# Kernel optimization log

Measured on AMD Instinct MI355X. Metric: run time of the kernel, lower is better.

## Reference

```python
import jax, jax.numpy as jnp
import numpy as np

BN_EPS = 1e-5
LRELU_SLOPE = 0.2


def setup_inputs() -> dict:
    key = jax.random.key(0)
    ks = jax.random.split(key, 8)
    B, N, D = 32, 2048, 64      # batch, nodes per graph, latent_dim
    E = 1_000_000               # num edges
    H = 128                     # edge_hidden_dim
    Din = 2 * D + 4             # concat(z_src, z_dst, edge_attr)
    z = jax.random.normal(ks[0], (B, N, D), dtype=jnp.float32)
    edge_index = jax.random.randint(ks[1], (2, E), 0, B * N, dtype=jnp.int64)
    edge_attr = jax.random.normal(ks[2], (E, 4), dtype=jnp.float32)
    W1 = jax.random.normal(ks[3], (Din, H), dtype=jnp.float32) * (1.0 / np.sqrt(Din))
    b1 = jnp.zeros((H,), dtype=jnp.float32)
    gamma = jnp.ones((H,), dtype=jnp.float32)
    beta = jnp.zeros((H,), dtype=jnp.float32)
    W2 = jax.random.normal(ks[4], (H, 1), dtype=jnp.float32) * (1.0 / np.sqrt(H))
    b2 = jnp.zeros((1,), dtype=jnp.float32)
    return {"z": z, "edge_attr": edge_attr, "W1": W1, "b1": b1,
            "gamma": gamma, "beta": beta, "W2": W2, "b2": b2,
            "edge_index": edge_index}


def reference(z, edge_attr, W1, b1, gamma, beta, W2, b2, edge_index):
    B, N, D = z.shape
    zf = z.reshape(-1, D)                       # [B*N, D]
    src, dst = edge_index[0], edge_index[1]
    edge_batch = jnp.clip(src // N, 0, B - 1)
    edge_offsets = edge_batch * N               # batch_offsets[edge_batch]
    src_idx = src % N + edge_offsets
    dst_idx = dst % N + edge_offsets
    edge_input = jnp.concatenate([zf[src_idx], zf[dst_idx], edge_attr], axis=1)  # [E, 2D+4]
    h = edge_input @ W1 + b1                    # [E, H]
    # BatchNorm1d (training mode: biased batch stats over edge dim)
    mu = jnp.mean(h, axis=0)
    var = jnp.mean(jnp.square(h - mu), axis=0)
    h = (h - mu) * jax.lax.rsqrt(var + BN_EPS) * gamma + beta
    h = jnp.where(h >= 0, h, LRELU_SLOPE * h)   # LeakyReLU(0.2)
    return h @ W2 + b2                          # [E, 1]
```

## Files before the change

kernel.cpp:

```cpp
#include <hip/hip_runtime.h>

#define E_EDGES   1000000
#define NNODES    2048
#define HCH       128
#define KP        136
#define TILE      64
#define NTILES    (E_EDGES / TILE)
#define NSPREAD   8
#define GRID_GEMM 1024
#define BPB       128
#define ZVEC      (32 * 2048 * 64 / 4)
#define ZBLK      2048
#define WBLK      66
#define NBIN      8
#define CBLK      512

typedef short  shortx8 __attribute__((ext_vector_type(8)));
typedef float  floatx4 __attribute__((ext_vector_type(4)));

__device__ __forceinline__ unsigned short f2bf(float f) {
  union { float f; unsigned int u; } v; v.f = f;
  unsigned int r = (v.u + 0x7fffu + ((v.u >> 16) & 1u)) >> 16;
  return (unsigned short)r;
}
__device__ __forceinline__ void cfence() { asm volatile("" ::: "memory"); }
__device__ __forceinline__ void bar_lds() {
  asm volatile("s_waitcnt lgkmcnt(0)" ::: "memory");
  __builtin_amdgcn_s_barrier();
  cfence();
}
__device__ __forceinline__ unsigned pack_rows(int s, int d) {
  unsigned rs = (unsigned)s & 0xFFFFu;
  unsigned rd = (unsigned)(((s & ~(NNODES - 1)) | (d & (NNODES - 1)))) & 0xFFFFu;
  return rs | (rd << 16);
}

__global__ void k_prep(const float* __restrict__ z, const float* __restrict__ W1,
                       const float* __restrict__ b1, const int* __restrict__ ei,
                       unsigned short* __restrict__ zb, unsigned short* __restrict__ w1t,
                       float* __restrict__ gstats, int* __restrict__ cnt) {
  int bid = blockIdx.x;
  if (bid < ZBLK) {
    const float4* z4 = (const float4*)z;
    ushort4* zb4 = (ushort4*)zb;
    for (int i = bid * 256 + threadIdx.x; i < ZVEC; i += ZBLK * 256) {
      float4 v = z4[i];
      ushort4 o;
      o.x = f2bf(v.x); o.y = f2bf(v.y); o.z = f2bf(v.z); o.w = f2bf(v.w);
      zb4[i] = o;
    }
  } else if (bid < ZBLK + WBLK) {
    int idx = (bid - ZBLK) * 256 + threadIdx.x;
    int k = idx >> 7, n = idx & 127;
    w1t[n * KP + k] = f2bf(W1[idx]);
  } else if (bid == ZBLK + WBLK) {
    int tid = threadIdx.x;
    if (tid < 512) {
      int n = tid >> 2, kp = 132 + (tid & 3);
      w1t[n * KP + kp] = (kp == 132) ? f2bf(b1[n]) : (unsigned short)0;
    }
    for (int i = tid; i < NSPREAD * 2 * HCH; i += 256) gstats[i] = 0.f;
  } else {
    __shared__ int lh[NBIN];
    int tid = threadIdx.x;
    int cb = bid - (ZBLK + WBLK + 1);
    if (tid < NBIN) lh[tid] = 0;
    __syncthreads();
    for (int e = cb * 256 + tid; e < E_EDGES; e += CBLK * 256)
      atomicAdd(&lh[((unsigned)ei[e]) >> 13], 1);
    __syncthreads();
    if (tid < NBIN) cnt[cb * NBIN + tid] = lh[tid];
  }
}

__global__ void k_scan(const int* __restrict__ cnt, int* __restrict__ base,
                       int* __restrict__ binTile) {
  __shared__ int tot[NBIN], S[NBIN + 1];
  int b = threadIdx.x;
  if (b < NBIN) {
    int t = 0;
    for (int blk = 0; blk < CBLK; ++blk) t += cnt[blk * NBIN + b];
    tot[b] = t;
  }
  __syncthreads();
  if (b == 0) {
    int a = 0;
    for (int i = 0; i < NBIN; ++i) { S[i] = a; a += tot[i]; }
    S[NBIN] = a;
    binTile[0] = 0;
    for (int i = 1; i <= NBIN; ++i) binTile[i] = (S[i] + 63) >> 6;
  }
  __syncthreads();
  if (b < NBIN) {
    int run = S[b];
    for (int blk = 0; blk < CBLK; ++blk) {
      base[blk * NBIN + b] = run;
      run += cnt[blk * NBIN + b];
    }
  }
}

__global__ __launch_bounds__(256)
void k_scatter(const int* __restrict__ ei, const float* __restrict__ attr,
               const int* __restrict__ base, uint4* __restrict__ recs) {
  __shared__ int lcnt[NBIN];
  int tid = threadIdx.x, bid = blockIdx.x;
  if (tid < NBIN) lcnt[tid] = base[bid * NBIN + tid];
  __syncthreads();
  for (int e = bid * 256 + tid; e < E_EDGES; e += CBLK * 256) {
    int s = ei[e], d = ei[E_EDGES + e];
    float4 a = ((const float4*)attr)[e];
    int b = ((unsigned)s) >> 13;
    int slot = atomicAdd(&lcnt[b], 1);
    uint4 r;
    r.x = pack_rows(s, d);
    r.y = (unsigned)f2bf(a.x) | ((unsigned)f2bf(a.y) << 16);
    r.z = (unsigned)f2bf(a.z) | ((unsigned)f2bf(a.w) << 16);
    r.w = (unsigned)e;
    recs[slot] = r;
  }
}

template<bool OUT>
__global__ __launch_bounds__(256, 4)
void k_gemm(const unsigned short* __restrict__ zb,
            const unsigned short* __restrict__ w1t,
            const uint4* __restrict__ recs,
            const int* __restrict__ binTile,
            float* __restrict__ gstats,
            const float* __restrict__ gamma,
            const float* __restrict__ beta,
            const float* __restrict__ W2,
            const float* __restrict__ b2,
            float* __restrict__ out) {
  __shared__ __align__(16) unsigned short A[2][TILE * KP];
  __shared__ float po[2][4][TILE];
  __shared__ int ostash[3][TILE];

  const int tid  = threadIdx.x;
  const int lane = tid & 63;
  const int w    = tid >> 6;
  const int l15  = lane & 15;
  const int quad = lane >> 4;
  const int ea   = w * 8 + (lane >> 3);
  const int eb   = ea + 32;
  const int ch   = lane & 7;

  shortx8 bfr[2][4], bfr4[2];
#pragma unroll
  for (int nt = 0; nt < 2; ++nt) {
    const unsigned short* bp = w1t + (w * 32 + nt * 16 + l15) * KP;
#pragma unroll
    for (int kk = 0; kk < 4; ++kk)
      bfr[nt][kk] = *(const shortx8*)(bp + kk * 32 + quad * 8);
    bfr4[nt] = (quad == 0) ? *(const shortx8*)(bp + 128)
                           : (shortx8){0, 0, 0, 0, 0, 0, 0, 0};
  }

  float eaf[2], ebb[2], ew2[2], b2v = 0.f;
  float ssum[2] = {0.f, 0.f}, ssq[2] = {0.f, 0.f};
  if (OUT) {
#pragma unroll
    for (int nt = 0; nt < 2; ++nt) {
      int c = w * 32 + nt * 16 + l15;
      float S = 0.f, Q = 0.f;
#pragma unroll
      for (int i = 0; i < NSPREAD; ++i) {
        S += gstats[i * 2 * HCH + c];
        Q += gstats[i * 2 * HCH + HCH + c];
      }
      float mu   = S * (1.0f / (float)E_EDGES);
      float var  = Q * (1.0f / (float)E_EDGES) - mu * mu;
      float rstd = rsqrtf(var + 1e-5f);
      float a = gamma[c] * rstd;
      eaf[nt] = a;
      ebb[nt] = beta[c] - mu * a;
      ew2[nt] = W2[c];
    }
    b2v = b2[0];
  }

  if (tid < 128) {
    int b = tid >> 6, r = tid & 63;
    ushort4 bl; bl.x = 0x3F80; bl.y = 0; bl.z = 0; bl.w = 0;
    *(ushort4*)(&A[b][0] + r * KP + 132) = bl;
  }

  const int x    = blockIdx.x & 7;
  const int t0i  = binTile[x] + (blockIdx.x >> 3);
  const int tEnd = binTile[x + 1];
  if (t0i >= tEnd) return;

  auto stage = [&](uint4 ra, uint4 rb, const uint4& h0, const uint4& h1,
                   const uint4& h2, const uint4& h3, int buf, int os) {
    *(uint4*)(&A[buf][0] + ea * KP + ch * 8)      = h0;
    *(uint4*)(&A[buf][0] + eb * KP + ch * 8)      = h1;
    *(uint4*)(&A[buf][0] + ea * KP + 64 + ch * 8) = h2;
    *(uint4*)(&A[buf][0] + eb * KP + 64 + ch * 8) = h3;
    if (ch == 0) {
      ushort4 aA; aA.x = (unsigned short)ra.y; aA.y = (unsigned short)(ra.y >> 16);
      aA.z = (unsigned short)ra.z; aA.w = (unsigned short)(ra.z >> 16);
      *(ushort4*)(&A[buf][0] + ea * KP + 128) = aA;
      ushort4 aB; aB.x = (unsigned short)rb.y; aB.y = (unsigned short)(rb.y >> 16);
      aB.z = (unsigned short)rb.z; aB.w = (unsigned short)(rb.z >> 16);
      *(ushort4*)(&A[buf][0] + eb * KP + 128) = aB;
      ostash[os][ea] = (int)ra.w;
      ostash[os][eb] = (int)rb.w;
    }
  };

  uint4 g0, g1, g2, g3;
  uint4 recSa, recSb;
  uint4 recFa, recFb;
  {
    uint4 ra = recs[t0i * TILE + ea];
    uint4 rb = recs[t0i * TILE + eb];
    unsigned r0 = ra.x & 0xFFFFu, r1 = rb.x & 0xFFFFu;
    unsigned r2 = ra.x >> 16,     r3 = rb.x >> 16;
    uint4 h0 = *(const uint4*)(zb + (size_t)r0 * 64 + ch * 8);
    uint4 h1 = *(const uint4*)(zb + (size_t)r1 * 64 + ch * 8);
    uint4 h2 = *(const uint4*)(zb + (size_t)r2 * 64 + ch * 8);
    uint4 h3 = *(const uint4*)(zb + (size_t)r3 * 64 + ch * 8);
    stage(ra, rb, h0, h1, h2, h3, 0, 0);
    int t1 = t0i + BPB; if (t1 > tEnd - 1) t1 = tEnd - 1;
    recSa = recs[t1 * TILE + ea];
    recSb = recs[t1 * TILE + eb];
    r0 = recSa.x & 0xFFFFu; r1 = recSb.x & 0xFFFFu;
    r2 = recSa.x >> 16;     r3 = recSb.x >> 16;
    g0 = *(const uint4*)(zb + (size_t)r0 * 64 + ch * 8);
    g1 = *(const uint4*)(zb + (size_t)r1 * 64 + ch * 8);
    g2 = *(const uint4*)(zb + (size_t)r2 * 64 + ch * 8);
    g3 = *(const uint4*)(zb + (size_t)r3 * 64 + ch * 8);
    int t2 = t0i + 2 * BPB; if (t2 > tEnd - 1) t2 = tEnd - 1;
    recFa = recs[t2 * TILE + ea];
    recFb = recs[t2 * TILE + eb];
  }
  bar_lds();

  int pp = 0, sl = 0, osr = 0;
  for (int tile = t0i; ; ) {
    const int tnext = tile + BPB;
    const bool more = tnext < tEnd;
    const int osw = (osr == 2) ? 0 : osr + 1;

    if (more) {
      stage(recSa, recSb, g0, g1, g2, g3, pp ^ 1, osw);
      unsigned r0 = recFa.x & 0xFFFFu, r1 = recFb.x & 0xFFFFu;
      unsigned r2 = recFa.x >> 16,     r3 = recFb.x >> 16;
      g0 = *(const uint4*)(zb + (size_t)r0 * 64 + ch * 8);
      g1 = *(const uint4*)(zb + (size_t)r1 * 64 + ch * 8);
      g2 = *(const uint4*)(zb + (size_t)r2 * 64 + ch * 8);
      g3 = *(const uint4*)(zb + (size_t)r3 * 64 + ch * 8);
      recSa = recFa; recSb = recFb;
      int tn3 = tile + 3 * BPB; if (tn3 > tEnd - 1) tn3 = tEnd - 1;
      recFa = recs[tn3 * TILE + ea];
      recFb = recs[tn3 * TILE + eb];
    }

    const unsigned short* Ar = &A[pp][0];
#pragma unroll
    for (int mt = 0; mt < 4; ++mt) {
      const unsigned short* ap = Ar + (mt * 16 + l15) * KP;
      shortx8 afr[4], a4;
#pragma unroll
      for (int kk = 0; kk < 4; ++kk)
        afr[kk] = *(const shortx8*)(ap + kk * 32 + quad * 8);
      a4 = (quad == 0) ? *(const shortx8*)(ap + 128)
                       : (shortx8){0, 0, 0, 0, 0, 0, 0, 0};

      floatx4 acc[2];
      acc[0] = (floatx4){0.f, 0.f, 0.f, 0.f};
      acc[1] = (floatx4){0.f, 0.f, 0.f, 0.f};
#pragma unroll
      for (int kk = 0; kk < 4; ++kk)
#pragma unroll
        for (int nt = 0; nt < 2; ++nt)
          acc[nt] = __builtin_amdgcn_mfma_f32_16x16x32_bf16(
              afr[kk], bfr[nt][kk], acc[nt], 0, 0, 0);
#pragma unroll
      for (int nt = 0; nt < 2; ++nt)
        acc[nt] = __builtin_amdgcn_mfma_f32_16x16x32_bf16(
            a4, bfr4[nt], acc[nt], 0, 0, 0);

      if (!OUT) {
#pragma unroll
        for (int nt = 0; nt < 2; ++nt) {
          float s = 0.f, qq = 0.f;
#pragma unroll
          for (int r = 0; r < 4; ++r) {
            float h = acc[nt][r];
            s += h; qq += h * h;
          }
          ssum[nt] += s; ssq[nt] += qq;
        }
      } else {
#pragma unroll
        for (int r = 0; r < 4; ++r) {
          float t = 0.f;
#pragma unroll
          for (int nt = 0; nt < 2; ++nt) {
            float h = acc[nt][r];
            float p = fmaf(eaf[nt], h, ebb[nt]);
            p = (p >= 0.f) ? p : 0.2f * p;
            t = fmaf(ew2[nt], p, t);
          }
          t += __shfl_xor(t, 1);
          t += __shfl_xor(t, 2);
          t += __shfl_xor(t, 4);
          t += __shfl_xor(t, 8);
          if (l15 == 0)
            po[sl][w][mt * 16 + quad * 4 + r] = t;
        }
      }
    }

    if (more || OUT) bar_lds();

    if (OUT && tid < TILE)
      out[ostash[osr][tid]] = po[sl][0][tid] + po[sl][1][tid] +
                              po[sl][2][tid] + po[sl][3][tid] + b2v;

    if (!more) break;
    pp ^= 1; sl ^= 1; osr = osw;
    tile = tnext;
  }

  if (!OUT) {
    float* gs = gstats + (blockIdx.x & (NSPREAD - 1)) * 2 * HCH;
#pragma unroll
    for (int nt = 0; nt < 2; ++nt) {
      float s = ssum[nt], qq = ssq[nt];
      s += __shfl_xor(s, 16); s += __shfl_xor(s, 32);
      qq += __shfl_xor(qq, 16); qq += __shfl_xor(qq, 32);
      if (quad == 0) {
        int c = w * 32 + nt * 16 + l15;
        atomicAdd(&gs[c], s);
        atomicAdd(&gs[HCH + c], qq);
      }
    }
  }
}

extern "C" void kernel_launch(void* const* d_in, const int* in_sizes, int n_in,
                              void* d_out, int out_size, void* d_ws, size_t ws_size,
                              hipStream_t stream) {
  const float* z     = (const float*)d_in[0];
  const float* attr  = (const float*)d_in[1];
  const float* W1    = (const float*)d_in[2];
  const float* b1    = (const float*)d_in[3];
  const float* gamma = (const float*)d_in[4];
  const float* beta  = (const float*)d_in[5];
  const float* W2    = (const float*)d_in[6];
  const float* b2    = (const float*)d_in[7];
  const int*   ei    = (const int*)d_in[8];
  float* out = (float*)d_out;

  char* ws = (char*)d_ws;
  unsigned short* zb  = (unsigned short*)ws;
  unsigned short* w1t = (unsigned short*)(ws + 8388608);
  float* gstats       = (float*)(ws + 8423424);
  int* cnt            = (int*)(ws + 8431616);
  int* base           = (int*)(ws + 8448000);
  int* binTile        = (int*)(ws + 8464384);
  uint4* recs         = (uint4*)(ws + 8464448);

  k_prep<<<ZBLK + WBLK + 1 + CBLK, 256, 0, stream>>>(z, W1, b1, ei, zb, w1t,
                                                     gstats, cnt);
  k_scan<<<1, 64, 0, stream>>>(cnt, base, binTile);
  k_scatter<<<CBLK, 256, 0, stream>>>(ei, attr, base, recs);
  k_gemm<false><<<GRID_GEMM, 256, 0, stream>>>(zb, w1t, recs, binTile, gstats,
                                               gamma, beta, W2, b2, nullptr);
  k_gemm<true><<<GRID_GEMM, 256, 0, stream>>>(zb, w1t, recs, binTile, gstats,
                                              gamma, beta, W2, b2, out);
}
```

Before: 261.5 us.

## Load gathered z rows directly into MFMA registers, drop LDS staging

```diff
diff --git a/kernel.cpp b/kernel.cpp
--- a/kernel.cpp
+++ b/kernel.cpp
@@ -23,12 +23,6 @@
   unsigned int r = (v.u + 0x7fffu + ((v.u >> 16) & 1u)) >> 16;
   return (unsigned short)r;
 }
-__device__ __forceinline__ void cfence() { asm volatile("" ::: "memory"); }
-__device__ __forceinline__ void bar_lds() {
-  asm volatile("s_waitcnt lgkmcnt(0)" ::: "memory");
-  __builtin_amdgcn_s_barrier();
-  cfence();
-}
 __device__ __forceinline__ unsigned pack_rows(int s, int d) {
   unsigned rs = (unsigned)s & 0xFFFFu;
   unsigned rd = (unsigned)(((s & ~(NNODES - 1)) | (d & (NNODES - 1)))) & 0xFFFFu;
@@ -38,7 +32,8 @@
 __global__ void k_prep(const float* __restrict__ z, const float* __restrict__ W1,
                        const float* __restrict__ b1, const int* __restrict__ ei,
                        unsigned short* __restrict__ zb, unsigned short* __restrict__ w1t,
-                       float* __restrict__ gstats, int* __restrict__ cnt) {
+                       float* __restrict__ gstats, int* __restrict__ cnt,
+                       float* __restrict__ out) {
   int bid = blockIdx.x;
   if (bid < ZBLK) {
     const float4* z4 = (const float4*)z;
@@ -49,6 +44,9 @@
       o.x = f2bf(v.x); o.y = f2bf(v.y); o.z = f2bf(v.z); o.w = f2bf(v.w);
       zb4[i] = o;
     }
+    float4 zf = {0.f, 0.f, 0.f, 0.f};
+    float4* o4 = (float4*)out;
+    for (int i = bid * 256 + threadIdx.x; i < (E_EDGES / 4); i += ZBLK * 256) o4[i] = zf;
   } else if (bid < ZBLK + WBLK) {
     int idx = (bid - ZBLK) * 256 + threadIdx.x;
     int k = idx >> 7, n = idx & 127;
@@ -133,18 +131,11 @@
             const float* __restrict__ W2,
             const float* __restrict__ b2,
             float* __restrict__ out) {
-  __shared__ __align__(16) unsigned short A[2][TILE * KP];
-  __shared__ float po[2][4][TILE];
-  __shared__ int ostash[3][TILE];
-
   const int tid  = threadIdx.x;
   const int lane = tid & 63;
   const int w    = tid >> 6;
   const int l15  = lane & 15;
   const int quad = lane >> 4;
-  const int ea   = w * 8 + (lane >> 3);
-  const int eb   = ea + 32;
-  const int ch   = lane & 7;
 
   shortx8 bfr[2][4], bfr4[2];
 #pragma unroll
@@ -177,13 +168,7 @@
       ebb[nt] = beta[c] - mu * a;
       ew2[nt] = W2[c];
     }
-    b2v = b2[0];
-  }
-
-  if (tid < 128) {
-    int b = tid >> 6, r = tid & 63;
-    ushort4 bl; bl.x = 0x3F80; bl.y = 0; bl.z = 0; bl.w = 0;
-    *(ushort4*)(&A[b][0] + r * KP + 132) = bl;
+    b2v = (w == 0) ? b2[0] : 0.f;
   }
 
   const int x    = blockIdx.x & 7;
@@ -191,138 +176,83 @@
   const int tEnd = binTile[x + 1];
   if (t0i >= tEnd) return;
 
-  auto stage = [&](uint4 ra, uint4 rb, const uint4& h0, const uint4& h1,
-                   const uint4& h2, const uint4& h3, int buf, int os) {
-    *(uint4*)(&A[buf][0] + ea * KP + ch * 8)      = h0;
-    *(uint4*)(&A[buf][0] + eb * KP + ch * 8)      = h1;
-    *(uint4*)(&A[buf][0] + ea * KP + 64 + ch * 8) = h2;
-    *(uint4*)(&A[buf][0] + eb * KP + 64 + ch * 8) = h3;
-    if (ch == 0) {
-      ushort4 aA; aA.x = (unsigned short)ra.y; aA.y = (unsigned short)(ra.y >> 16);
-      aA.z = (unsigned short)ra.z; aA.w = (unsigned short)(ra.z >> 16);
-      *(ushort4*)(&A[buf][0] + ea * KP + 128) = aA;
-      ushort4 aB; aB.x = (unsigned short)rb.y; aB.y = (unsigned short)(rb.y >> 16);
-      aB.z = (unsigned short)rb.z; aB.w = (unsigned short)(rb.z >> 16);
-      *(ushort4*)(&A[buf][0] + eb * KP + 128) = aB;
-      ostash[os][ea] = (int)ra.w;
-      ostash[os][eb] = (int)rb.w;
-    }
+  const char* zq = (const char*)zb + quad * 16;
+
+  auto zload = [&](uint4 rec, uint4* zf) {
+    unsigned so = (rec.x & 0xFFFFu) << 7;
+    unsigned dofs = (rec.x >> 16) << 7;
+    zf[0] = *(const uint4*)(zq + so);
+    zf[1] = *(const uint4*)(zq + so + 64);
+    zf[2] = *(const uint4*)(zq + dofs);
+    zf[3] = *(const uint4*)(zq + dofs + 64);
   };
 
-  uint4 g0, g1, g2, g3;
-  uint4 recSa, recSb;
-  uint4 recFa, recFb;
-  {
-    uint4 ra = recs[t0i * TILE + ea];
-    uint4 rb = recs[t0i * TILE + eb];
-    unsigned r0 = ra.x & 0xFFFFu, r1 = rb.x & 0xFFFFu;
-    unsigned r2 = ra.x >> 16,     r3 = rb.x >> 16;
-    uint4 h0 = *(const uint4*)(zb + (size_t)r0 * 64 + ch * 8);
-    uint4 h1 = *(const uint4*)(zb + (size_t)r1 * 64 + ch * 8);
-    uint4 h2 = *(const uint4*)(zb + (size_t)r2 * 64 + ch * 8);
-    uint4 h3 = *(const uint4*)(zb + (size_t)r3 * 64 + ch * 8);
-    stage(ra, rb, h0, h1, h2, h3, 0, 0);
-    int t1 = t0i + BPB; if (t1 > tEnd - 1) t1 = tEnd - 1;
-    recSa = recs[t1 * TILE + ea];
-    recSb = recs[t1 * TILE + eb];
-    r0 = recSa.x & 0xFFFFu; r1 = recSb.x & 0xFFFFu;
-    r2 = recSa.x >> 16;     r3 = recSb.x >> 16;
-    g0 = *(const uint4*)(zb + (size_t)r0 * 64 + ch * 8);
-    g1 = *(const uint4*)(zb + (size_t)r1 * 64 + ch * 8);
-    g2 = *(const uint4*)(zb + (size_t)r2 * 64 + ch * 8);
-    g3 = *(const uint4*)(zb + (size_t)r3 * 64 + ch * 8);
-    int t2 = t0i + 2 * BPB; if (t2 > tEnd - 1) t2 = tEnd - 1;
-    recFa = recs[t2 * TILE + ea];
-    recFb = recs[t2 * TILE + eb];
-  }
-  bar_lds();
-
-  int pp = 0, sl = 0, osr = 0;
-  for (int tile = t0i; ; ) {
-    const int tnext = tile + BPB;
-    const bool more = tnext < tEnd;
-    const int osw = (osr == 2) ? 0 : osr + 1;
-
-    if (more) {
-      stage(recSa, recSb, g0, g1, g2, g3, pp ^ 1, osw);
-      unsigned r0 = recFa.x & 0xFFFFu, r1 = recFb.x & 0xFFFFu;
-      unsigned r2 = recFa.x >> 16,     r3 = recFb.x >> 16;
-      g0 = *(const uint4*)(zb + (size_t)r0 * 64 + ch * 8);
-      g1 = *(const uint4*)(zb + (size_t)r1 * 64 + ch * 8);
-      g2 = *(const uint4*)(zb + (size_t)r2 * 64 + ch * 8);
-      g3 = *(const uint4*)(zb + (size_t)r3 * 64 + ch * 8);
-      recSa = recFa; recSb = recFb;
-      int tn3 = tile + 3 * BPB; if (tn3 > tEnd - 1) tn3 = tEnd - 1;
-      recFa = recs[tn3 * TILE + ea];
-      recFb = recs[tn3 * TILE + eb];
-    }
-
-    const unsigned short* Ar = &A[pp][0];
-#pragma unroll
-    for (int mt = 0; mt < 4; ++mt) {
-      const unsigned short* ap = Ar + (mt * 16 + l15) * KP;
-      shortx8 afr[4], a4;
-#pragma unroll
-      for (int kk = 0; kk < 4; ++kk)
-        afr[kk] = *(const shortx8*)(ap + kk * 32 + quad * 8);
-      a4 = (quad == 0) ? *(const shortx8*)(ap + 128)
-                       : (shortx8){0, 0, 0, 0, 0, 0, 0, 0};
-
-      floatx4 acc[2];
-      acc[0] = (floatx4){0.f, 0.f, 0.f, 0.f};
-      acc[1] = (floatx4){0.f, 0.f, 0.f, 0.f};
-#pragma unroll
-      for (int kk = 0; kk < 4; ++kk)
-#pragma unroll
-        for (int nt = 0; nt < 2; ++nt)
-          acc[nt] = __builtin_amdgcn_mfma_f32_16x16x32_bf16(
-              afr[kk], bfr[nt][kk], acc[nt], 0, 0, 0);
+  auto do_mt = [&](uint4 rec, const uint4* zf, int tile, int mt) {
+    int4 ai;
+    if (quad == 0) { ai.x = (int)rec.y; ai.y = (int)rec.z; ai.z = 0x3F80; ai.w = 0; }
+    else           { ai.x = 0; ai.y = 0; ai.z = 0; ai.w = 0; }
+    shortx8 a4; __builtin_memcpy(&a4, &ai, 16);
+
+    floatx4 acc[2];
+    acc[0] = (floatx4){0.f, 0.f, 0.f, 0.f};
+    acc[1] = (floatx4){0.f, 0.f, 0.f, 0.f};
+#pragma unroll
+    for (int kk = 0; kk < 4; ++kk) {
+      shortx8 afr; __builtin_memcpy(&afr, &zf[kk], 16);
 #pragma unroll
       for (int nt = 0; nt < 2; ++nt)
         acc[nt] = __builtin_amdgcn_mfma_f32_16x16x32_bf16(
-            a4, bfr4[nt], acc[nt], 0, 0, 0);
-
-      if (!OUT) {
+            afr, bfr[nt][kk], acc[nt], 0, 0, 0);
+    }
+#pragma unroll
+    for (int nt = 0; nt < 2; ++nt)
+      acc[nt] = __builtin_amdgcn_mfma_f32_16x16x32_bf16(
+          a4, bfr4[nt], acc[nt], 0, 0, 0);
+
+    if (!OUT) {
+#pragma unroll
+      for (int nt = 0; nt < 2; ++nt) {
+        float s = 0.f, qq = 0.f;
+#pragma unroll
+        for (int r = 0; r < 4; ++r) {
+          float h = acc[nt][r];
+          s += h; qq += h * h;
+        }
+        ssum[nt] += s; ssq[nt] += qq;
+      }
+    } else {
+#pragma unroll
+      for (int r = 0; r < 4; ++r) {
+        float t = 0.f;
 #pragma unroll
         for (int nt = 0; nt < 2; ++nt) {
-          float s = 0.f, qq = 0.f;
-#pragma unroll
-          for (int r = 0; r < 4; ++r) {
-            float h = acc[nt][r];
-            s += h; qq += h * h;
-          }
-          ssum[nt] += s; ssq[nt] += qq;
+          float h = acc[nt][r];
+          float p = fmaf(eaf[nt], h, ebb[nt]);
+          p = fmaxf(p, 0.2f * p);
+          t = fmaf(ew2[nt], p, t);
         }
-      } else {
-#pragma unroll
-        for (int r = 0; r < 4; ++r) {
-          float t = 0.f;
-#pragma unroll
-          for (int nt = 0; nt < 2; ++nt) {
-            float h = acc[nt][r];
-            float p = fmaf(eaf[nt], h, ebb[nt]);
-            p = (p >= 0.f) ? p : 0.2f * p;
-            t = fmaf(ew2[nt], p, t);
-          }
-          t += __shfl_xor(t, 1);
-          t += __shfl_xor(t, 2);
-          t += __shfl_xor(t, 4);
-          t += __shfl_xor(t, 8);
-          if (l15 == 0)
-            po[sl][w][mt * 16 + quad * 4 + r] = t;
-        }
+        t += __shfl_xor(t, 1);
+        t += __shfl_xor(t, 2);
+        t += __shfl_xor(t, 4);
+        t += __shfl_xor(t, 8);
+        int og = __shfl((int)rec.w, quad * 4 + r);
+        if (l15 == 0) atomicAdd(&out[og], t + b2v);
       }
     }
-
-    if (more || OUT) bar_lds();
-
-    if (OUT && tid < TILE)
-      out[ostash[osr][tid]] = po[sl][0][tid] + po[sl][1][tid] +
-                              po[sl][2][tid] + po[sl][3][tid] + b2v;
-
-    if (!more) break;
-    pp ^= 1; sl ^= 1; osr = osw;
-    tile = tnext;
+  };
+
+  for (int tile = t0i; tile < tEnd; tile += BPB) {
+    const uint4* rt = recs + tile * TILE + l15;
+    uint4 r0 = rt[0], r1 = rt[16], r2 = rt[32], r3 = rt[48];
+    uint4 za[4], zc[4];
+    zload(r0, za);
+    zload(r1, zc);
+    do_mt(r0, za, tile, 0);
+    zload(r2, za);
+    do_mt(r1, zc, tile, 1);
+    zload(r3, zc);
+    do_mt(r2, za, tile, 2);
+    do_mt(r3, zc, tile, 3);
   }
 
   if (!OUT) {
@@ -365,7 +295,7 @@
   uint4* recs         = (uint4*)(ws + 8464448);
 
   k_prep<<<ZBLK + WBLK + 1 + CBLK, 256, 0, stream>>>(z, W1, b1, ei, zb, w1t,
-                                                     gstats, cnt);
+                                                     gstats, cnt, out);
   k_scan<<<1, 64, 0, stream>>>(cnt, base, binTile);
   k_scatter<<<CBLK, 256, 0, stream>>>(ei, attr, base, recs);
   k_gemm<false><<<GRID_GEMM, 256, 0, stream>>>(zb, w1t, recs, binTile, gstats,
```

New measurement: 481.7 us. +84.2%, slower.
